# Kernel tuning notes

Measured on AMD Instinct MI355X. Metric: run time of the kernel, lower is better.

## Reference

```python
import jax, jax.numpy as jnp
import numpy as np

B, T, D, H = 64, 1024, 300, 512
Hd = H // 2  # per-direction GRU hidden size


def setup_inputs() -> dict:
    key = jax.random.key(0)
    ks = jax.random.split(key, 12)
    s = 0.05
    return {
        "x": jax.random.normal(ks[0], (B, T, D), jnp.float32),
        "lengths": jax.random.randint(ks[1], (B,), 1, T + 1, jnp.int32),
        # forward-direction GRU params (torch layout: [3*Hd, in])
        "w_ih_f": jax.random.normal(ks[2], (3 * Hd, D), jnp.float32) * s,
        "w_hh_f": jax.random.normal(ks[3], (3 * Hd, Hd), jnp.float32) * s,
        "b_ih_f": jax.random.normal(ks[4], (3 * Hd,), jnp.float32) * s,
        "b_hh_f": jax.random.normal(ks[5], (3 * Hd,), jnp.float32) * s,
        # backward-direction GRU params
        "w_ih_b": jax.random.normal(ks[6], (3 * Hd, D), jnp.float32) * s,
        "w_hh_b": jax.random.normal(ks[7], (3 * Hd, Hd), jnp.float32) * s,
        "b_ih_b": jax.random.normal(ks[8], (3 * Hd,), jnp.float32) * s,
        "b_hh_b": jax.random.normal(ks[9], (3 * Hd,), jnp.float32) * s,
        # attention: hidden layer [H, H] + bias, context vector [H] (no bias)
        "att_w": jax.random.normal(ks[10], (H, H), jnp.float32) * s,
        "att_b": jnp.zeros((H,), jnp.float32),
        "ctx_v": jax.random.normal(ks[11], (H,), jnp.float32) * s,
    }


def _gru_dir(x, w_ih, w_hh, b_ih, b_hh):
    """Single-direction GRU over padded [B,T,D] input, h0=0. Torch gate math."""
    gx = jnp.einsum("btd,gd->btg", x, w_ih) + b_ih  # [B,T,3Hd], big GEMM up front

    def step(h, gx_t):
        gh = h @ w_hh.T + b_hh
        xr, xz, xn = jnp.split(gx_t, 3, axis=-1)
        hr, hz, hn = jnp.split(gh, 3, axis=-1)
        r = jax.nn.sigmoid(xr + hr)
        z = jax.nn.sigmoid(xz + hz)
        n = jnp.tanh(xn + r * hn)
        h = (1.0 - z) * n + z * h
        return h, h

    h0 = jnp.zeros((x.shape[0], w_hh.shape[1]), x.dtype)
    _, hs = jax.lax.scan(step, h0, jnp.swapaxes(gx, 0, 1))  # [T,B,Hd]
    return jnp.swapaxes(hs, 0, 1)  # [B,T,Hd]


def _forward(x, lengths, w_ih_f, w_hh_f, b_ih_f, b_hh_f,
             w_ih_b, w_hh_b, b_ih_b, b_hh_b, att_w, att_b, ctx_v):
    mask = jnp.arange(T)[None, :] < lengths[:, None]  # [B,T]
    xm = x * mask[..., None].astype(x.dtype)  # original pads sequences with 0
    # bidirectional GRU: backward dir runs over the full padded sequence
    # (zeros included), exactly like the original padded nn.GRU call.
    enc_f = _gru_dir(xm, w_ih_f, w_hh_f, b_ih_f, b_hh_f)
    enc_b = _gru_dir(xm[:, ::-1], w_ih_b, w_hh_b, b_ih_b, b_hh_b)[:, ::-1]
    enc = jnp.concatenate([enc_f, enc_b], axis=-1)  # [B,T,H]
    # attention: tanh hidden layer -> context vector -> masked softmax over T
    u = jnp.tanh(jnp.einsum("bth,oh->bto", enc, att_w) + att_b)
    logits = jnp.einsum("bth,h->bt", u, ctx_v)
    logits = jnp.where(mask, logits, -jnp.inf)
    att = jax.nn.softmax(logits, axis=-1)  # pad positions get exact 0 weight
    return jnp.einsum("bt,bth->bh", att, enc)  # weighted sum pooling -> [B,H]


def reference(x, lengths, w_ih_f, w_hh_f, b_ih_f, b_hh_f,
              w_ih_b, w_hh_b, b_ih_b, b_hh_b, att_w, att_b, ctx_v):
    return _forward(x, lengths, w_ih_f, w_hh_f, b_ih_f, b_hh_f,
                    w_ih_b, w_hh_b, b_ih_b, b_hh_b, att_w, att_b, ctx_v)
```

## Files before the change

kernel.cpp:

```cpp
#include <hip/hip_runtime.h>

#define T_SEQ 1024
#define BATCH 64
#define DIN   300
#define DPAD  320
#define HD    256
#define NW    1536
#define ROWS  65536

typedef _Float16 f16x8 __attribute__((ext_vector_type(8)));
typedef _Float16 h2_t  __attribute__((ext_vector_type(2)));
typedef float    f32x4 __attribute__((ext_vector_type(4)));

__device__ __forceinline__ float dot2f(h2_t a, h2_t b, float c) {
#if __has_builtin(__builtin_amdgcn_fdot2)
    return __builtin_amdgcn_fdot2(a, b, c, false);
#else
    return c + (float)a[0]*(float)b[0] + (float)a[1]*(float)b[1];
#endif
}

__device__ __forceinline__ float sigmoidf_(float x) { return 1.f/(1.f+__expf(-x)); }
__device__ __forceinline__ float tanhf_(float x)    { return 1.f - 2.f/(__expf(2.f*x)+1.f); }

__global__ void prep_x(const float* __restrict__ x, const int* __restrict__ len,
                       _Float16* __restrict__ xh) {
    int r = blockIdx.x, k = threadIdx.x;
    int b = r >> 10, t = r & 1023;
    float v = (k < DIN && t < len[b]) ? x[(size_t)r*DIN + k] : 0.f;
    xh[(size_t)r*DPAD + k] = (_Float16)v;
}

__global__ void prep_w(const float* __restrict__ wihf, const float* __restrict__ wihb,
                       const float* __restrict__ bihf, const float* __restrict__ bihb,
                       const float* __restrict__ attw,
                       _Float16* __restrict__ wih, _Float16* __restrict__ attwh,
                       float* __restrict__ bih) {
    int bid = blockIdx.x, tid = threadIdx.x;
    if (bid < NW) {
        const float* src = (bid < 768) ? (wihf + (size_t)bid*DIN)
                                       : (wihb + (size_t)(bid-768)*DIN);
        if (tid < DPAD)
            wih[(size_t)bid*DPAD + tid] = (_Float16)((tid < DIN) ? src[tid] : 0.f);
        if (tid == 0)
            bih[bid] = (bid < 768) ? bihf[bid] : bihb[bid-768];
    } else {
        int n = bid - NW;
        attwh[(size_t)n*512 + tid] = (_Float16)attw[(size_t)n*512 + tid];
    }
}

__global__ __launch_bounds__(256) void gemm_gx(const _Float16* __restrict__ xh,
                                               const _Float16* __restrict__ wih,
                                               const float* __restrict__ bih,
                                               _Float16* __restrict__ gx) {
    int m0 = blockIdx.x * 64, n0 = blockIdx.y * 128;
    __shared__ _Float16 As[64][40];
    __shared__ _Float16 Bs[128][40];
    int tid = threadIdx.x;
    int wave = tid >> 6, lane = tid & 63;
    f32x4 acc[8] = {};
    for (int kt = 0; kt < 10; ++kt) {
        int k0 = kt * 32;
        {
            int r = tid >> 2, ko = (tid & 3) * 8;
            *(f16x8*)&As[r][ko] = *(const f16x8*)&xh[(size_t)(m0+r)*DPAD + k0 + ko];
        }
        {
            int r = tid >> 1, ko = (tid & 1) * 16;
            *(f16x8*)&Bs[r][ko]   = *(const f16x8*)&wih[(size_t)(n0+r)*DPAD + k0 + ko];
            *(f16x8*)&Bs[r][ko+8] = *(const f16x8*)&wih[(size_t)(n0+r)*DPAD + k0 + ko + 8];
        }
        __syncthreads();
        int kk = (lane >> 4) * 8;
        f16x8 a = *(const f16x8*)&As[wave*16 + (lane & 15)][kk];
#pragma unroll
        for (int nf = 0; nf < 8; ++nf) {
            f16x8 bfr = *(const f16x8*)&Bs[nf*16 + (lane & 15)][kk];
            acc[nf] = __builtin_amdgcn_mfma_f32_16x16x32_f16(a, bfr, acc[nf], 0, 0, 0);
        }
        __syncthreads();
    }
#pragma unroll
    for (int nf = 0; nf < 8; ++nf) {
        int n = n0 + nf*16 + (lane & 15);
        float bv = bih[n];
#pragma unroll
        for (int r = 0; r < 4; ++r) {
            int m = m0 + wave*16 + (lane >> 4)*4 + r;
            gx[(size_t)m*NW + n] = (_Float16)(acc[nf][r] + bv);
        }
    }
}

__global__ __launch_bounds__(512, 2) void gru_kernel(
        const float* __restrict__ whhf, const float* __restrict__ whhb,
        const float* __restrict__ bhhf, const float* __restrict__ bhhb,
        const _Float16* __restrict__ gx, _Float16* __restrict__ enc) {
    int bid = blockIdx.x;
    int dir = bid & 1, b = bid >> 1;
    int tid = threadIdx.x;
    int j = tid >> 1;
    int half = tid & 1;
    const float* whh = dir ? whhb : whhf;
    const float* bhh = dir ? bhhb : bhhf;

    h2_t wr[64], wz[64], wn[64];
    {
        const float2* pr = (const float2*)(whh + (size_t)j*HD        + half*128);
        const float2* pz = (const float2*)(whh + (size_t)(HD + j)*HD + half*128);
        const float2* pn = (const float2*)(whh + (size_t)(2*HD+j)*HD + half*128);
#pragma unroll
        for (int k2 = 0; k2 < 64; ++k2) {
            float2 a = pr[k2]; wr[k2] = h2_t{(_Float16)a.x, (_Float16)a.y};
            float2 c = pz[k2]; wz[k2] = h2_t{(_Float16)c.x, (_Float16)c.y};
            float2 d = pn[k2]; wn[k2] = h2_t{(_Float16)d.x, (_Float16)d.y};
        }
    }
    float brh = half ? 0.f : bhh[j];
    float bzh = half ? 0.f : bhh[HD + j];
    float bnh = half ? 0.f : bhh[2*HD + j];

    __shared__ __align__(16) _Float16 hbuf[2][HD];
    if (tid < HD) hbuf[0][tid] = (_Float16)0.f;
    float hprev = 0.f;
    __syncthreads();

    const _Float16* gxb = gx + (size_t)b*T_SEQ*NW + dir*768 + j;
    int t = dir ? (T_SEQ - 1) : 0;
    int dt = dir ? -1 : 1;
    const _Float16* gp0 = gxb + (size_t)t*NW;
    float xr = (float)gp0[0], xz = (float)gp0[HD], xn = (float)gp0[2*HD];
    int cur = 0;

    for (int s = 0; s < T_SEQ; ++s) {
        float nxr = 0.f, nxz = 0.f, nxn = 0.f;
        if (s + 1 < T_SEQ) {
            const _Float16* gq = gxb + (size_t)(t + dt)*NW;
            nxr = (float)gq[0]; nxz = (float)gq[HD]; nxn = (float)gq[2*HD];
        }

        float hr0 = brh, hz0 = bzh, hn0 = bnh;
        float hr1 = 0.f, hz1 = 0.f, hn1 = 0.f;
        const _Float16* hb = &hbuf[cur][half*128];
#pragma unroll
        for (int k = 0; k < 16; ++k) {
            f16x8 hv = *(const f16x8*)&hb[k*8];
            h2_t a0 = {hv[0], hv[1]}, a1 = {hv[2], hv[3]};
            h2_t a2 = {hv[4], hv[5]}, a3 = {hv[6], hv[7]};
            hr0 = dot2f(a0, wr[4*k+0], hr0); hr1 = dot2f(a1, wr[4*k+1], hr1);
            hr0 = dot2f(a2, wr[4*k+2], hr0); hr1 = dot2f(a3, wr[4*k+3], hr1);
            hz0 = dot2f(a0, wz[4*k+0], hz0); hz1 = dot2f(a1, wz[4*k+1], hz1);
            hz0 = dot2f(a2, wz[4*k+2], hz0); hz1 = dot2f(a3, wz[4*k+3], hz1);
            hn0 = dot2f(a0, wn[4*k+0], hn0); hn1 = dot2f(a1, wn[4*k+1], hn1);
            hn0 = dot2f(a2, wn[4*k+2], hn0); hn1 = dot2f(a3, wn[4*k+3], hn1);
        }
        float hr = hr0 + hr1, hz = hz0 + hz1, hn = hn0 + hn1;
        hr += __shfl_xor(hr, 1);
        hz += __shfl_xor(hz, 1);
        hn += __shfl_xor(hn, 1);

        float r  = sigmoidf_(xr + hr);
        float z  = sigmoidf_(xz + hz);
        float nn = tanhf_(xn + r * hn);
        float h  = (1.f - z) * nn + z * hprev;
        hprev = h;
        if (!half) {
            enc[((size_t)(b*T_SEQ + t))*512 + dir*HD + j] = (_Float16)h;
            hbuf[cur ^ 1][j] = (_Float16)h;
        }
        __syncthreads();
        xr = nxr; xz = nxz; xn = nxn;
        cur ^= 1; t += dt;
    }
}

__global__ __launch_bounds__(256) void gemm_u(const _Float16* __restrict__ enc,
                                              const _Float16* __restrict__ attwh,
                                              const float* __restrict__ attb,
                                              const float* __restrict__ ctx,
                                              float* __restrict__ logits) {
    int m0 = blockIdx.x * 64;
    __shared__ _Float16 As[64][40];
    __shared__ _Float16 Bs[512][40];
    int tid = threadIdx.x;
    int wave = tid >> 6, lane = tid & 63;
    f32x4 acc[32] = {};
    for (int kt = 0; kt < 16; ++kt) {
        int k0 = kt * 32;
        {
            int r = tid >> 2, ko = (tid & 3) * 8;
            *(f16x8*)&As[r][ko] = *(const f16x8*)&enc[(size_t)(m0+r)*512 + k0 + ko];
        }
        {
#pragma unroll
            for (int jr = 0; jr < 2; ++jr) {
                int row = tid*2 + jr;
#pragma unroll
                for (int q = 0; q < 4; ++q)
                    *(f16x8*)&Bs[row][q*8] =
                        *(const f16x8*)&attwh[(size_t)row*512 + k0 + q*8];
            }
        }
        __syncthreads();
        int kk = (lane >> 4) * 8;
        f16x8 a = *(const f16x8*)&As[wave*16 + (lane & 15)][kk];
#pragma unroll
        for (int nf = 0; nf < 32; ++nf) {
            f16x8 bfr = *(const f16x8*)&Bs[nf*16 + (lane & 15)][kk];
            acc[nf] = __builtin_amdgcn_mfma_f32_16x16x32_f16(a, bfr, acc[nf], 0, 0, 0);
        }
        __syncthreads();
    }
    float rs0 = 0.f, rs1 = 0.f, rs2 = 0.f, rs3 = 0.f;
#pragma unroll
    for (int nf = 0; nf < 32; ++nf) {
        int n = nf*16 + (lane & 15);
        float bv = attb[n], cv = ctx[n];
        rs0 += tanhf_(acc[nf][0] + bv) * cv;
        rs1 += tanhf_(acc[nf][1] + bv) * cv;
        rs2 += tanhf_(acc[nf][2] + bv) * cv;
        rs3 += tanhf_(acc[nf][3] + bv) * cv;
    }
#pragma unroll
    for (int off = 1; off < 16; off <<= 1) {
        rs0 += __shfl_xor(rs0, off);
        rs1 += __shfl_xor(rs1, off);
        rs2 += __shfl_xor(rs2, off);
        rs3 += __shfl_xor(rs3, off);
    }
    if ((lane & 15) == 0) {
        int mb = m0 + wave*16 + (lane >> 4)*4;
        logits[mb + 0] = rs0;
        logits[mb + 1] = rs1;
        logits[mb + 2] = rs2;
        logits[mb + 3] = rs3;
    }
}

__global__ __launch_bounds__(256) void softmax_pool(const float* __restrict__ logits,
                                                    const _Float16* __restrict__ enc,
                                                    const int* __restrict__ lengths,
                                                    float* __restrict__ out) {
    int b = blockIdx.x, tid = threadIdx.x;
    int len = lengths[b];
    if (len < 1) len = 1;
    if (len > T_SEQ) len = T_SEQ;
    __shared__ float att[T_SEQ];
    __shared__ float red[8];
    const float* lg = logits + (size_t)b*T_SEQ;

    float m = -1e30f;
    for (int t = tid; t < len; t += 256) m = fmaxf(m, lg[t]);
#pragma unroll
    for (int off = 1; off < 64; off <<= 1) m = fmaxf(m, __shfl_xor(m, off));
    if ((tid & 63) == 0) red[tid >> 6] = m;
    __syncthreads();
    m = fmaxf(fmaxf(red[0], red[1]), fmaxf(red[2], red[3]));

    float s = 0.f;
    for (int t = tid; t < len; t += 256) {
        float e = __expf(lg[t] - m);
        att[t] = e;
        s += e;
    }
#pragma unroll
    for (int off = 1; off < 64; off <<= 1) s += __shfl_xor(s, off);
    if ((tid & 63) == 0) red[4 + (tid >> 6)] = s;
    __syncthreads();
    s = red[4] + red[5] + red[6] + red[7];
    float inv = 1.f / s;

    float a0 = 0.f, a1 = 0.f;
    const _Float16* eb = enc + (size_t)b*T_SEQ*512;
    for (int t = 0; t < len; ++t) {
        float w = att[t];
        a0 += w * (float)eb[(size_t)t*512 + tid];
        a1 += w * (float)eb[(size_t)t*512 + 256 + tid];
    }
    out[(size_t)b*512 + tid]       = a0 * inv;
    out[(size_t)b*512 + 256 + tid] = a1 * inv;
}

extern "C" void kernel_launch(void* const* d_in, const int* in_sizes, int n_in,
                              void* d_out, int out_size, void* d_ws, size_t ws_size,
                              hipStream_t stream) {
    const float* x    = (const float*)d_in[0];
    const int*   len  = (const int*)  d_in[1];
    const float* wihf = (const float*)d_in[2];
    const float* whhf = (const float*)d_in[3];
    const float* bihf = (const float*)d_in[4];
    const float* bhhf = (const float*)d_in[5];
    const float* wihb = (const float*)d_in[6];
    const float* whhb = (const float*)d_in[7];
    const float* bihb = (const float*)d_in[8];
    const float* bhhb = (const float*)d_in[9];
    const float* attw = (const float*)d_in[10];
    const float* attb = (const float*)d_in[11];
    const float* ctxv = (const float*)d_in[12];
    float* out = (float*)d_out;

    char* ws = (char*)d_ws;
    size_t off = 0;
    _Float16* xh    = (_Float16*)(ws + off); off += (size_t)ROWS*DPAD*2;
    _Float16* wih   = (_Float16*)(ws + off); off += (size_t)NW*DPAD*2;
    _Float16* attwh = (_Float16*)(ws + off); off += (size_t)512*512*2;
    float*    bih   = (float*)   (ws + off); off += (size_t)NW*4;
    _Float16* gx    = (_Float16*)(ws + off); off += (size_t)ROWS*NW*2;
    _Float16* enc   = (_Float16*)(ws + off); off += (size_t)ROWS*512*2;
    float*    logit = (float*)   (ws + off); off += (size_t)ROWS*4;

    prep_x<<<dim3(ROWS), dim3(DPAD), 0, stream>>>(x, len, xh);
    prep_w<<<dim3(NW + 512), dim3(512), 0, stream>>>(wihf, wihb, bihf, bihb, attw,
                                                     wih, attwh, bih);
    gemm_gx<<<dim3(ROWS/64, NW/128), dim3(256), 0, stream>>>(xh, wih, bih, gx);
    gru_kernel<<<dim3(2*BATCH), dim3(512), 0, stream>>>(whhf, whhb, bhhf, bhhb, gx, enc);
    gemm_u<<<dim3(ROWS/64), dim3(256), 0, stream>>>(enc, attwh, attb, ctxv, logit);
    softmax_pool<<<dim3(BATCH), dim3(256), 0, stream>>>(logit, enc, len, out);
}
```

Measured before the change: 1.723 ms.

## Split GRU recurrent dot products across four lanes per hidden unit

The recurrent GRU kernel moves from 512 to 1024 threads per block. Each hidden unit's three 256-long dot products are now split across four lanes instead of two, which halves the serial dot2 chain per thread and the register-resident weights. The partial sums are combined with two xor-shuffle rounds. The shared hidden-state buffer is split into four padded 64-element segments, and paired lanes write two fp16 outputs at once to shared memory and to enc. The cost is an extra shuffle round per step and more waves taking part in each per-step block barrier.

```diff
diff --git a/kernel.cpp b/kernel.cpp
--- a/kernel.cpp
+++ b/kernel.cpp
@@ -93,36 +93,40 @@
     }
 }
 
-__global__ __launch_bounds__(512, 2) void gru_kernel(
+__global__ void __launch_bounds__(1024)
+gru_kernel(
         const float* __restrict__ whhf, const float* __restrict__ whhb,
         const float* __restrict__ bhhf, const float* __restrict__ bhhb,
         const _Float16* __restrict__ gx, _Float16* __restrict__ enc) {
     int bid = blockIdx.x;
     int dir = bid & 1, b = bid >> 1;
     int tid = threadIdx.x;
-    int j = tid >> 1;
-    int half = tid & 1;
+    int j = tid >> 2;
+    int q = tid & 3;
     const float* whh = dir ? whhb : whhf;
     const float* bhh = dir ? bhhb : bhhf;
 
-    h2_t wr[64], wz[64], wn[64];
+    h2_t wr[32], wz[32], wn[32];
     {
-        const float2* pr = (const float2*)(whh + (size_t)j*HD        + half*128);
-        const float2* pz = (const float2*)(whh + (size_t)(HD + j)*HD + half*128);
-        const float2* pn = (const float2*)(whh + (size_t)(2*HD+j)*HD + half*128);
-#pragma unroll
-        for (int k2 = 0; k2 < 64; ++k2) {
-            float2 a = pr[k2]; wr[k2] = h2_t{(_Float16)a.x, (_Float16)a.y};
-            float2 c = pz[k2]; wz[k2] = h2_t{(_Float16)c.x, (_Float16)c.y};
-            float2 d = pn[k2]; wn[k2] = h2_t{(_Float16)d.x, (_Float16)d.y};
-        }
-    }
-    float brh = half ? 0.f : bhh[j];
-    float bzh = half ? 0.f : bhh[HD + j];
-    float bnh = half ? 0.f : bhh[2*HD + j];
-
-    __shared__ __align__(16) _Float16 hbuf[2][HD];
-    if (tid < HD) hbuf[0][tid] = (_Float16)0.f;
+        const float2* pr = (const float2*)(whh + (size_t)j*HD        + q*64);
+        const float2* pz = (const float2*)(whh + (size_t)(HD + j)*HD + q*64);
+        const float2* pn = (const float2*)(whh + (size_t)(2*HD+j)*HD + q*64);
+#pragma unroll
+        for (int k = 0; k < 32; ++k) { float2 a = pr[k]; wr[k] = h2_t{(_Float16)a.x, (_Float16)a.y}; }
+#pragma unroll
+        for (int k = 0; k < 32; ++k) { float2 a = pz[k]; wz[k] = h2_t{(_Float16)a.x, (_Float16)a.y}; }
+#pragma unroll
+        for (int k = 0; k < 32; ++k) { float2 a = pn[k]; wn[k] = h2_t{(_Float16)a.x, (_Float16)a.y}; }
+    }
+    float brh = (q == 0) ? bhh[j]        : 0.f;
+    float bzh = (q == 0) ? bhh[HD + j]   : 0.f;
+    float bnh = (q == 0) ? bhh[2*HD + j] : 0.f;
+
+    __shared__ __align__(16) _Float16 hb[2][4][72];
+    {
+        _Float16* hz0 = &hb[0][0][0];
+        if (tid < 2*4*72) hz0[tid] = (_Float16)0.f;
+    }
     float hprev = 0.f;
     __syncthreads();
 
@@ -140,34 +144,36 @@
             nxr = (float)gq[0]; nxz = (float)gq[HD]; nxn = (float)gq[2*HD];
         }
 
-        float hr0 = brh, hz0 = bzh, hn0 = bnh;
-        float hr1 = 0.f, hz1 = 0.f, hn1 = 0.f;
-        const _Float16* hb = &hbuf[cur][half*128];
-#pragma unroll
-        for (int k = 0; k < 16; ++k) {
-            f16x8 hv = *(const f16x8*)&hb[k*8];
+        float ar = brh, az = bzh, an = bnh;
+        float ar1 = 0.f, az1 = 0.f, an1 = 0.f;
+        const _Float16* hseg = &hb[cur][q][0];
+#pragma unroll
+        for (int k8 = 0; k8 < 8; ++k8) {
+            f16x8 hv = *(const f16x8*)&hseg[k8*8];
             h2_t a0 = {hv[0], hv[1]}, a1 = {hv[2], hv[3]};
             h2_t a2 = {hv[4], hv[5]}, a3 = {hv[6], hv[7]};
-            hr0 = dot2f(a0, wr[4*k+0], hr0); hr1 = dot2f(a1, wr[4*k+1], hr1);
-            hr0 = dot2f(a2, wr[4*k+2], hr0); hr1 = dot2f(a3, wr[4*k+3], hr1);
-            hz0 = dot2f(a0, wz[4*k+0], hz0); hz1 = dot2f(a1, wz[4*k+1], hz1);
-            hz0 = dot2f(a2, wz[4*k+2], hz0); hz1 = dot2f(a3, wz[4*k+3], hz1);
-            hn0 = dot2f(a0, wn[4*k+0], hn0); hn1 = dot2f(a1, wn[4*k+1], hn1);
-            hn0 = dot2f(a2, wn[4*k+2], hn0); hn1 = dot2f(a3, wn[4*k+3], hn1);
-        }
-        float hr = hr0 + hr1, hz = hz0 + hz1, hn = hn0 + hn1;
-        hr += __shfl_xor(hr, 1);
-        hz += __shfl_xor(hz, 1);
-        hn += __shfl_xor(hn, 1);
+            ar = dot2f(a0, wr[4*k8+0], ar); ar1 = dot2f(a1, wr[4*k8+1], ar1);
+            ar = dot2f(a2, wr[4*k8+2], ar); ar1 = dot2f(a3, wr[4*k8+3], ar1);
+            az = dot2f(a0, wz[4*k8+0], az); az1 = dot2f(a1, wz[4*k8+1], az1);
+            az = dot2f(a2, wz[4*k8+2], az); az1 = dot2f(a3, wz[4*k8+3], az1);
+            an = dot2f(a0, wn[4*k8+0], an); an1 = dot2f(a1, wn[4*k8+1], an1);
+            an = dot2f(a2, wn[4*k8+2], an); an1 = dot2f(a3, wn[4*k8+3], an1);
+        }
+        float hr = ar + ar1, hzv = az + az1, hn = an + an1;
+        hr += __shfl_xor(hr, 1); hzv += __shfl_xor(hzv, 1); hn += __shfl_xor(hn, 1);
+        hr += __shfl_xor(hr, 2); hzv += __shfl_xor(hzv, 2); hn += __shfl_xor(hn, 2);
 
         float r  = sigmoidf_(xr + hr);
-        float z  = sigmoidf_(xz + hz);
+        float z  = sigmoidf_(xz + hzv);
         float nn = tanhf_(xn + r * hn);
         float h  = (1.f - z) * nn + z * hprev;
         hprev = h;
-        if (!half) {
-            enc[((size_t)(b*T_SEQ + t))*512 + dir*HD + j] = (_Float16)h;
-            hbuf[cur ^ 1][j] = (_Float16)h;
+
+        float hpar = __shfl_xor(h, 4);
+        if ((tid & 7) == 0) {
+            h2_t hp = {(_Float16)h, (_Float16)hpar};
+            *(h2_t*)&hb[cur ^ 1][j >> 6][j & 63] = hp;
+            *(h2_t*)&enc[((size_t)(b*T_SEQ + t))*512 + dir*HD + j] = hp;
         }
         __syncthreads();
         xr = nxr; xz = nxz; xn = nxn;
@@ -314,7 +320,7 @@
     prep_w<<<dim3(NW + 512), dim3(512), 0, stream>>>(wihf, wihb, bihf, bihb, attw,
                                                      wih, attwh, bih);
     gemm_gx<<<dim3(ROWS/64, NW/128), dim3(256), 0, stream>>>(xh, wih, bih, gx);
-    gru_kernel<<<dim3(2*BATCH), dim3(512), 0, stream>>>(whhf, whhb, bhhf, bhhb, gx, enc);
+    gru_kernel<<<dim3(2*BATCH), dim3(1024), 0, stream>>>(whhf, whhb, bhhf, bhhb, gx, enc);
     gemm_u<<<dim3(ROWS/64), dim3(256), 0, stream>>>(enc, attwh, attb, ctxv, logit);
     softmax_pool<<<dim3(BATCH), dim3(256), 0, stream>>>(logit, enc, len, out);
 }
```

Result: slower. 2.310 ms (+34.1%).
